# Optimization experiments

Hardware: AMD Instinct MI355X
Metric: run time of the kernel (lower is better)

Reference implementation:

```python
import jax, jax.numpy as jnp
import numpy as np
from jax import lax

B, L, D = 4, 4096, 1024
EXP = 2
DI = D * EXP
K_PERC = 7
KS_DIFF = 3
DILATIONS = (1, 4, 16)


def _dwconv(h, w, dil):
    # h: [B, C, L] channels-first, w: [C, 1, k] depthwise kernel (groups=C)
    k = w.shape[-1]
    pad = dil * (k // 2)
    return lax.conv_general_dilated(
        h, w, window_strides=(1,), padding=[(pad, pad)],
        rhs_dilation=(dil,), dimension_numbers=("NCH", "OIH", "NCH"),
        feature_group_count=w.shape[0])


def _layernorm(x, g, b, eps=1e-5):
    m = jnp.mean(x, axis=-1, keepdims=True)
    v = jnp.mean(jnp.square(x - m), axis=-1, keepdims=True)
    return (x - m) * lax.rsqrt(v + eps) * g + b


def setup_inputs() -> dict:
    key = jax.random.key(0)
    ks = jax.random.split(key, 16)
    n = lambda k, shape, scale: (jax.random.normal(k, shape, dtype=jnp.float32) * scale)
    inp = {
        "x": n(ks[0], (B, L, D), 1.0),
        # PerceptionFilter: 3 depthwise convs k=7, pointwise 3D->D, LayerNorm
        "pf_w0": n(ks[1], (D, 1, K_PERC), 0.3),
        "pf_w1": n(ks[2], (D, 1, K_PERC), 0.3),
        "pf_w2": n(ks[3], (D, 1, K_PERC), 0.3),
        "pf_pw": n(ks[4], (D, 3 * D), 1.0 / np.sqrt(3 * D)),
        "ln_g": jnp.ones((D,), jnp.float32),
        "ln_b": jnp.zeros((D,), jnp.float32),
        # ReactionGate: wu/wg: 2D->DI, wd: DI->D, alpha
        "rg_wu": n(ks[5], (DI, 2 * D), 1.0 / np.sqrt(2 * D)),
        "rg_wg": n(ks[6], (DI, 2 * D), 1.0 / np.sqrt(2 * D)),
        "rg_wd": n(ks[7], (D, DI), 1.0 / np.sqrt(DI)),
        "rg_alpha": jnp.full((D,), 0.1, jnp.float32),
        # MultiRateDiffusion: 3 depthwise dilated convs k=3, selector D->3, strength
        "md_w0": n(ks[8], (D, 1, KS_DIFF), 0.3),
        "md_w1": n(ks[9], (D, 1, KS_DIFF), 0.3),
        "md_w2": n(ks[10], (D, 1, KS_DIFF), 0.3),
        "md_sel": n(ks[11], (len(DILATIONS), D), 1.0 / np.sqrt(D)),
        "md_strength": jnp.asarray(0.1, jnp.float32),
    }
    return inp


def reference(x, pf_w0, pf_w1, pf_w2, pf_pw, ln_g, ln_b,
              rg_wu, rg_wg, rg_wd, rg_alpha,
              md_w0, md_w1, md_w2, md_sel, md_strength):
    # --- PerceptionFilter ---
    h = jnp.swapaxes(x, 1, 2)  # [B, D, L]
    pcat = jnp.concatenate([_dwconv(h, w, 1) for w in (pf_w0, pf_w1, pf_w2)], axis=1)  # [B, 3D, L]
    p = jnp.einsum("bcl,dc->bld", pcat, pf_pw)  # pointwise 1x1 conv -> [B, L, D]
    p = _layernorm(p, ln_g, ln_b)
    # --- ReactionGate ---
    cat = jnp.concatenate([x, p], axis=-1)  # [B, L, 2D]
    u = cat @ rg_wu.T
    g = jax.nn.sigmoid(cat @ rg_wg.T)
    x2 = x + rg_alpha * ((g * jax.nn.silu(u)) @ rg_wd.T)
    # --- MultiRateDiffusion ---
    h2 = jnp.swapaxes(x2, 1, 2)  # [B, D, L]
    diffs = jnp.stack([_dwconv(h2, w, dil) for w, dil in
                       zip((md_w0, md_w1, md_w2), DILATIONS)], axis=-1)  # [B, D, L, R]
    wsel = jax.nn.softmax(x2 @ md_sel.T, axis=-1)[:, None]  # [B, 1, L, R]
    combined = jnp.swapaxes(jnp.sum(diffs * wsel, axis=-1), 1, 2)  # [B, L, D]
    return x2 + md_strength * (combined - x2)
```

## Files before the change

### kernel.cpp

```cpp
#include <hip/hip_runtime.h>

#define LL 4096
#define BL 16384

typedef __attribute__((ext_vector_type(4))) float f32x4;
typedef __attribute__((ext_vector_type(4))) int i32x4;
typedef __attribute__((ext_vector_type(4))) unsigned short u16x4;
typedef __attribute__((ext_vector_type(2))) int i32x2;
typedef unsigned short ushort_t;
typedef unsigned int u32;

static __device__ __forceinline__ unsigned short f2bf(float f) {
    union { float f; unsigned int i; } v; v.f = f;
    unsigned int r = v.i + 0x7fffu + ((v.i >> 16) & 1u);
    return (unsigned short)(r >> 16);
}
static __device__ __forceinline__ float bf2f(unsigned short u) {
    union { unsigned int i; float f; } v; v.i = ((unsigned int)u) << 16; return v.f;
}
static __device__ __forceinline__ int qclamp(float x, float s) {
    return (int)rintf(fminf(fmaxf(x * s, -127.f), 127.f));
}
static __device__ __forceinline__ int q4(float a, float b, float c, float d, float s) {
    return (qclamp(a,s) & 255) | ((qclamp(b,s) & 255) << 8) |
           ((qclamp(c,s) & 255) << 16) | ((qclamp(d,s) & 255) << 24);
}

static __device__ __forceinline__ i32x4 mfma_i8(i32x4 a, i32x4 b, i32x4 c) {
    asm("v_mfma_i32_16x16x64_i8 %0, %1, %2, %0" : "+v"(c) : "v"(a), "v"(b));
    return c;
}

static __device__ __forceinline__ void gload16(const char* g, char* l) {
    __builtin_amdgcn_global_load_lds(
        (const __attribute__((address_space(1))) u32*)g,
        (__attribute__((address_space(3))) u32*)l, 16, 0, 0);
}

#define BAR()   asm volatile("s_barrier" ::: "memory")
#define VMW0()  asm volatile("s_waitcnt vmcnt(0)" ::: "memory")

__global__ void cvt_w8(const float* __restrict__ in, char* __restrict__ out,
                       int n4, float s) {
    int i = blockIdx.x * blockDim.x + threadIdx.x;
    int stride = gridDim.x * blockDim.x;
    for (; i < n4; i += stride) {
        f32x4 v = ((const f32x4*)in)[i];
        ((int*)out)[i] = q4(v[0], v[1], v[2], v[3], s);
    }
}

__global__ __launch_bounds__(256) void cvt_wug8(
    const float* __restrict__ wu, const float* __restrict__ wg,
    char* __restrict__ wug, float s)
{
    int r = blockIdx.x;
    int type = (r >> 4) & 1;
    int src = ((r >> 5) << 4) | (r & 15);
    const float* sp = (type ? wg : wu) + (size_t)src * 2048;
    char* d = wug + (size_t)r * 2048;
    int i = threadIdx.x;
    f32x4 v0 = ((const f32x4*)sp)[2 * i];
    f32x4 v1 = ((const f32x4*)sp)[2 * i + 1];
    i32x2 o = { q4(v0[0], v0[1], v0[2], v0[3], s),
                q4(v1[0], v1[1], v1[2], v1[3], s) };
    ((i32x2*)d)[i] = o;
}

__global__ __launch_bounds__(256) void pf_conv(
    const float* __restrict__ x,
    const float* __restrict__ w0, const float* __restrict__ w1, const float* __restrict__ w2,
    char* __restrict__ pcat, char* __restrict__ cat, float sP, float sX)
{
    int bl = blockIdx.x;
    int b = bl >> 12;
    int l = bl & 4095;
    int c0 = threadIdx.x << 2;

    f32x4 v[7];
#pragma unroll
    for (int t = 0; t < 7; ++t) {
        int ls = l + t - 3;
        if (ls >= 0 && ls < LL)
            v[t] = *(const f32x4*)(x + (((size_t)b * LL + ls) << 10) + c0);
        else {
            f32x4 z = {0.f, 0.f, 0.f, 0.f};
            v[t] = z;
        }
    }
    *(int*)(cat + (((size_t)bl) << 11) + c0) = q4(v[3][0], v[3][1], v[3][2], v[3][3], sX);
    const float* ww[3] = { w0, w1, w2 };
#pragma unroll
    for (int j = 0; j < 3; ++j) {
        const float* w = ww[j];
        float a[4];
#pragma unroll
        for (int e = 0; e < 4; ++e) {
            int c = c0 + e;
            float s = 0.f;
#pragma unroll
            for (int t = 0; t < 7; ++t) s += v[t][e] * w[c * 7 + t];
            a[e] = s;
        }
        *(int*)(pcat + (size_t)bl * 3072 + j * 1024 + c0) = q4(a[0], a[1], a[2], a[3], sP);
    }
}

__global__ __launch_bounds__(256) void ln_kernel(
    const ushort_t* __restrict__ p, const float* __restrict__ g,
    const float* __restrict__ bta, char* __restrict__ cat, float sX)
{
    int bl = blockIdx.x;
    int tid = threadIdx.x;
    int c0 = tid << 2;
    u16x4 pv = *(const u16x4*)(p + (((size_t)bl) << 10) + c0);
    float v0 = bf2f(pv[0]), v1 = bf2f(pv[1]), v2 = bf2f(pv[2]), v3 = bf2f(pv[3]);
    float s  = v0 + v1 + v2 + v3;
    float sq = v0*v0 + v1*v1 + v2*v2 + v3*v3;
#pragma unroll
    for (int off = 32; off > 0; off >>= 1) {
        s  += __shfl_down(s, off);
        sq += __shfl_down(sq, off);
    }
    __shared__ float rs[4], rq[4];
    int w = tid >> 6;
    if ((tid & 63) == 0) { rs[w] = s; rq[w] = sq; }
    __syncthreads();
    float S = rs[0] + rs[1] + rs[2] + rs[3];
    float Q = rq[0] + rq[1] + rq[2] + rq[3];
    float m   = S * (1.f / 1024.f);
    float var = Q * (1.f / 1024.f) - m * m;
    float inv = rsqrtf(var + 1e-5f);
    f32x4 gv = *(const f32x4*)(g + c0);
    f32x4 bv = *(const f32x4*)(bta + c0);
    *(int*)(cat + (((size_t)bl) << 11) + 1024 + c0) =
        q4((v0-m)*inv*gv[0]+bv[0], (v1-m)*inv*gv[1]+bv[1],
           (v2-m)*inv*gv[2]+bv[2], (v3-m)*inv*gv[3]+bv[3], sX);
}

template<int MODE>
__global__ __launch_bounds__(256, 3) void gemm8i(
    const char* __restrict__ A, const char* __restrict__ Bm,
    ushort_t* __restrict__ C16, char* __restrict__ C8,
    float* __restrict__ Cf, const float* __restrict__ X,
    const float* __restrict__ alpha,
    int N, int K, int lgny, float invS, float sOut)
{
    __shared__ char smem[32768];
    const int tid = threadIdx.x;
    const int wid = tid >> 6, lane = tid & 63;
    const int fr = lane & 15, fq = lane >> 4;
    const int wm = (wid >> 1) * 64;
    const int wn = (wid & 1) * 64;

    const int nwg = gridDim.x * gridDim.y;
    const int orig = blockIdx.y * gridDim.x + blockIdx.x;
    const int q = nwg >> 3;
    const int tile = (orig & 7) * q + (orig >> 3);
    const int m0 = (tile >> lgny) * 128;
    const int n0 = (tile & ((1 << lgny) - 1)) * 128;

    const int sp_ = tid >> 3;
    const int ss_ = tid & 7;
    const char* gp[4];
    int lpo[4];
#pragma unroll
    for (int op = 0; op < 2; ++op)
#pragma unroll
        for (int j = 0; j < 2; ++j) {
            int idx = op * 2 + j;
            const char* gs = op ? Bm : A;
            int rb = op ? n0 : m0;
            int p = j * 32 + sp_;
            int sh = ss_ ^ (p & 7);
            int r = 2 * p + (sh >> 2);
            int cch = sh & 3;
            gp[idx] = gs + (size_t)(rb + r) * K + cch * 16;
            lpo[idx] = op * 8192 + p * 128 + ss_ * 16;
        }

    const int lo = (fr >> 1) * 128 + (((((fr & 1) << 2) | fq)) ^ (fr >> 1)) * 16;
    const int arow = wm * 64 + lo;
    const int brow = 8192 + wn * 64 + lo;

    i32x4 acc[4][4] = {};
    const int NT = K >> 6;

#define STAGE(kt, s_) do {                                                  \
    _Pragma("unroll") for (int i_ = 0; i_ < 4; ++i_)                        \
        gload16(gp[i_] + (size_t)(kt) * 64, smem + (s_) * 16384 + lpo[i_]); \
    } while (0)

    STAGE(0, 0);
    VMW0();
    BAR();

    for (int t = 0; t < NT; ++t) {
        const int s = t & 1;
        const char* base = smem + s * 16384;
        const bool st = (t + 1 < NT);

        if (st) STAGE(t + 1, s ^ 1);

        i32x4 b[4], a[4];
#pragma unroll
        for (int n_ = 0; n_ < 4; ++n_) b[n_] = *(const i32x4*)(base + brow + n_ * 1024);
#pragma unroll
        for (int i_ = 0; i_ < 4; ++i_) a[i_] = *(const i32x4*)(base + arow + i_ * 1024);
        __builtin_amdgcn_s_setprio(1);
#pragma unroll
        for (int i_ = 0; i_ < 4; ++i_)
#pragma unroll
            for (int n_ = 0; n_ < 4; ++n_)
                acc[i_][n_] = mfma_i8(a[i_], b[n_], acc[i_][n_]);
        __builtin_amdgcn_s_setprio(0);

        if (st) VMW0();
        BAR();
    }
#undef STAGE

    const int mbase = m0 + wm + fq * 4;
#pragma unroll
    for (int mi = 0; mi < 4; ++mi) {
        if (MODE == 1) {
#pragma unroll
            for (int pi = 0; pi < 2; ++pi)
#pragma unroll
                for (int r = 0; r < 4; ++r) {
                    float u = (float)acc[mi][2 * pi][r] * invS;
                    float g = (float)acc[mi][2 * pi + 1][r] * invS;
                    float sg = 1.f / (1.f + __expf(-g));
                    float sl = u / (1.f + __expf(-u));
                    int col = ((n0 + wn) >> 1) + pi * 16 + fr;
                    C8[(size_t)(mbase + mi * 16 + r) * (N >> 1) + col] =
                        (char)qclamp(sg * sl, sOut);
                }
        } else {
#pragma unroll
            for (int ni = 0; ni < 4; ++ni)
#pragma unroll
                for (int r = 0; r < 4; ++r) {
                    int row = mbase + mi * 16 + r;
                    int col = n0 + wn + ni * 16 + fr;
                    size_t idx = (size_t)row * N + col;
                    float vv = (float)acc[mi][ni][r] * invS;
                    if (MODE == 0) C16[idx] = f2bf(vv);
                    else           Cf[idx] = X[idx] + alpha[col] * vv;
                }
        }
    }
}

__global__ __launch_bounds__(256) void diffusion(
    const float* __restrict__ x2,
    const float* __restrict__ w0, const float* __restrict__ w1, const float* __restrict__ w2,
    const float* __restrict__ sel, const float* __restrict__ strength_p,
    float* __restrict__ out)
{
    int bl = blockIdx.x;
    int b = bl >> 12;
    int l = bl & 4095;
    int tid = threadIdx.x;
    int c0 = tid << 2;
    const float* base = x2 + (((size_t)b * LL) << 10);

    f32x4 xc = *(const f32x4*)(x2 + (((size_t)bl) << 10) + c0);
    f32x4 s0 = *(const f32x4*)(sel + c0);
    f32x4 s1 = *(const f32x4*)(sel + 1024 + c0);
    f32x4 s2 = *(const f32x4*)(sel + 2048 + c0);
    float t0 = xc[0]*s0[0] + xc[1]*s0[1] + xc[2]*s0[2] + xc[3]*s0[3];
    float t1 = xc[0]*s1[0] + xc[1]*s1[1] + xc[2]*s1[2] + xc[3]*s1[3];
    float t2 = xc[0]*s2[0] + xc[1]*s2[1] + xc[2]*s2[2] + xc[3]*s2[3];
#pragma unroll
    for (int off = 32; off > 0; off >>= 1) {
        t0 += __shfl_down(t0, off);
        t1 += __shfl_down(t1, off);
        t2 += __shfl_down(t2, off);
    }
    __shared__ float r0[4], r1[4], r2[4];
    int w = tid >> 6;
    if ((tid & 63) == 0) { r0[w] = t0; r1[w] = t1; r2[w] = t2; }
    __syncthreads();
    float L0 = r0[0] + r0[1] + r0[2] + r0[3];
    float L1 = r1[0] + r1[1] + r1[2] + r1[3];
    float L2 = r2[0] + r2[1] + r2[2] + r2[3];
    float mx = fmaxf(L0, fmaxf(L1, L2));
    float e0 = __expf(L0 - mx), e1 = __expf(L1 - mx), e2 = __expf(L2 - mx);
    float inv = 1.f / (e0 + e1 + e2);
    float ws0 = e0 * inv, ws1 = e1 * inv, ws2 = e2 * inv;
    float stg = *strength_p;

    f32x4 comb = {0.f, 0.f, 0.f, 0.f};
    const float* wset[3] = { w0, w1, w2 };
    const int dils[3] = { 1, 4, 16 };
    const float wsel[3] = { ws0, ws1, ws2 };
#pragma unroll
    for (int r = 0; r < 3; ++r) {
        const float* wp = wset[r] + (size_t)c0 * 3;
        float wf[12];
        *(f32x4*)&wf[0] = *(const f32x4*)(wp + 0);
        *(f32x4*)&wf[4] = *(const f32x4*)(wp + 4);
        *(f32x4*)&wf[8] = *(const f32x4*)(wp + 8);
        int dil = dils[r];
        f32x4 d = {0.f, 0.f, 0.f, 0.f};
#pragma unroll
        for (int t = 0; t < 3; ++t) {
            int ls = l + (t - 1) * dil;
            f32x4 xv;
            if (ls >= 0 && ls < LL)
                xv = *(const f32x4*)(base + (((size_t)ls) << 10) + c0);
            else {
                f32x4 z = {0.f, 0.f, 0.f, 0.f};
                xv = z;
            }
#pragma unroll
            for (int e = 0; e < 4; ++e) d[e] += xv[e] * wf[e * 3 + t];
        }
#pragma unroll
        for (int e = 0; e < 4; ++e) comb[e] += wsel[r] * d[e];
    }
    f32x4 o;
#pragma unroll
    for (int e = 0; e < 4; ++e) o[e] = xc[e] + stg * (comb[e] - xc[e]);
    *(f32x4*)(out + (((size_t)bl) << 10) + c0) = o;
}

extern "C" void kernel_launch(void* const* d_in, const int* in_sizes, int n_in,
                              void* d_out, int out_size, void* d_ws, size_t ws_size,
                              hipStream_t stream)
{
    const float* x      = (const float*)d_in[0];
    const float* pf_w0  = (const float*)d_in[1];
    const float* pf_w1  = (const float*)d_in[2];
    const float* pf_w2  = (const float*)d_in[3];
    const float* pf_pw  = (const float*)d_in[4];
    const float* ln_g   = (const float*)d_in[5];
    const float* ln_b   = (const float*)d_in[6];
    const float* rg_wu  = (const float*)d_in[7];
    const float* rg_wg  = (const float*)d_in[8];
    const float* rg_wd  = (const float*)d_in[9];
    const float* rg_al  = (const float*)d_in[10];
    const float* md_w0  = (const float*)d_in[11];
    const float* md_w1  = (const float*)d_in[12];
    const float* md_w2  = (const float*)d_in[13];
    const float* md_sel = (const float*)d_in[14];
    const float* md_str = (const float*)d_in[15];
    float* outp = (float*)d_out;

    const float sP  = 127.f / 5.f;
    const float sX  = 127.f / 6.f;
    const float sW1 = 127.f / 0.11f;
    const float sW  = 127.f / 0.14f;
    const float invS1 = 1.f / (sP * sW1);
    const float invS2 = 1.f / (sX * sW);

    char* ws = (char*)d_ws;
    size_t off = 0;
    char*     pcat8 = (char*)   (ws + off); off += (size_t)BL * 3072;
    char*     cat8  = (char*)   (ws + off); off += (size_t)BL * 2048;
    ushort_t* ppre  = (ushort_t*)(ws + off); off += (size_t)BL * 1024 * 2;
    float*    x2    = (float*)  (ws + off); off += (size_t)BL * 1024 * 4;
    char*     wpw8  = (char*)   (ws + off); off += (size_t)1024 * 3072;
    char*     wug8  = (char*)   (ws + off); off += (size_t)4096 * 2048;
    char*     wd8   = (char*)   (ws + off); off += (size_t)1024 * 2048;
    char*     act8  = pcat8;

    cvt_w8<<<256, 256, 0, stream>>>(pf_pw, wpw8, 1024 * 3072 / 4, sW1);
    cvt_w8<<<256, 256, 0, stream>>>(rg_wd, wd8, 1024 * 2048 / 4, sW);
    cvt_wug8<<<4096, 256, 0, stream>>>(rg_wu, rg_wg, wug8, sW);

    pf_conv<<<BL, 256, 0, stream>>>(x, pf_w0, pf_w1, pf_w2, pcat8, cat8, sP, sX);

    gemm8i<0><<<dim3(128, 8), 256, 0, stream>>>(
        pcat8, wpw8, ppre, nullptr, nullptr, nullptr, nullptr, 1024, 3072, 3, invS1, 0.f);

    ln_kernel<<<BL, 256, 0, stream>>>(ppre, ln_g, ln_b, cat8, sX);

    gemm8i<1><<<dim3(128, 32), 256, 0, stream>>>(
        cat8, wug8, nullptr, act8, nullptr, nullptr, nullptr, 4096, 2048, 5, invS2, sX);

    gemm8i<2><<<dim3(128, 8), 256, 0, stream>>>(
        act8, wd8, nullptr, nullptr, x2, x, rg_al, 1024, 2048, 3, invS2, 0.f);

    diffusion<<<BL, 256, 0, stream>>>(x2, md_w0, md_w1, md_w2, md_sel, md_str, outp);
}
```

Before: 529.0 us.

## Double the int8 GEMM K-tile to 128 with a new swizzled LDS layout

The int8 MFMA GEMM now stages 128-wide K slices instead of 64, using 64KB of double-buffered LDS and a simpler XOR row swizzle. Each iteration runs two rounds of MFMA and halves the number of barriers and loop iterations. The cost is lower occupancy: launch bounds drop from 3 to 2 blocks per CU, and more LDS is used per block.

```diff
diff --git a/kernel.cpp b/kernel.cpp
--- a/kernel.cpp
+++ b/kernel.cpp
@@ -139,14 +139,14 @@
 }
 
 template<int MODE>
-__global__ __launch_bounds__(256, 3) void gemm8i(
+__global__ __launch_bounds__(256, 2) void gemm8i(
     const char* __restrict__ A, const char* __restrict__ Bm,
     ushort_t* __restrict__ C16, char* __restrict__ C8,
     float* __restrict__ Cf, const float* __restrict__ X,
     const float* __restrict__ alpha,
     int N, int K, int lgny, float invS, float sOut)
 {
-    __shared__ char smem[32768];
+    __shared__ char smem[65536];
     const int tid = threadIdx.x;
     const int wid = tid >> 6, lane = tid & 63;
     const int fr = lane & 15, fq = lane >> 4;
@@ -160,35 +160,32 @@
     const int m0 = (tile >> lgny) * 128;
     const int n0 = (tile & ((1 << lgny) - 1)) * 128;
 
-    const int sp_ = tid >> 3;
-    const int ss_ = tid & 7;
-    const char* gp[4];
-    int lpo[4];
+    const int srow = tid >> 3;
+    const int gch = ((tid & 7) ^ (srow & 7)) * 16;
+    const char* gp[8];
+    int lpo[8];
 #pragma unroll
     for (int op = 0; op < 2; ++op)
 #pragma unroll
-        for (int j = 0; j < 2; ++j) {
-            int idx = op * 2 + j;
+        for (int j = 0; j < 4; ++j) {
+            int idx = op * 4 + j;
             const char* gs = op ? Bm : A;
             int rb = op ? n0 : m0;
-            int p = j * 32 + sp_;
-            int sh = ss_ ^ (p & 7);
-            int r = 2 * p + (sh >> 2);
-            int cch = sh & 3;
-            gp[idx] = gs + (size_t)(rb + r) * K + cch * 16;
-            lpo[idx] = op * 8192 + p * 128 + ss_ * 16;
-        }
-
-    const int lo = (fr >> 1) * 128 + (((((fr & 1) << 2) | fq)) ^ (fr >> 1)) * 16;
-    const int arow = wm * 64 + lo;
-    const int brow = 8192 + wn * 64 + lo;
+            gp[idx] = gs + (size_t)(rb + j * 32 + srow) * K + gch;
+            lpo[idx] = op * 16384 + (j * 32 + srow) * 128 + (tid & 7) * 16;
+        }
+
+    const int ach0 = (fq ^ (fr & 7)) * 16;
+    const int ach1 = ((4 + fq) ^ (fr & 7)) * 16;
+    const int arow = (wm + fr) * 128;
+    const int brow = 16384 + (wn + fr) * 128;
 
     i32x4 acc[4][4] = {};
-    const int NT = K >> 6;
+    const int NT = K >> 7;
 
 #define STAGE(kt, s_) do {                                                  \
-    _Pragma("unroll") for (int i_ = 0; i_ < 4; ++i_)                        \
-        gload16(gp[i_] + (size_t)(kt) * 64, smem + (s_) * 16384 + lpo[i_]); \
+    _Pragma("unroll") for (int i_ = 0; i_ < 8; ++i_)                        \
+        gload16(gp[i_] + (size_t)(kt) * 128, smem + (s_) * 32768 + lpo[i_]);\
     } while (0)
 
     STAGE(0, 0);
@@ -197,16 +194,27 @@
 
     for (int t = 0; t < NT; ++t) {
         const int s = t & 1;
-        const char* base = smem + s * 16384;
+        const char* base = smem + s * 32768;
         const bool st = (t + 1 < NT);
 
         if (st) STAGE(t + 1, s ^ 1);
 
         i32x4 b[4], a[4];
 #pragma unroll
-        for (int n_ = 0; n_ < 4; ++n_) b[n_] = *(const i32x4*)(base + brow + n_ * 1024);
-#pragma unroll
-        for (int i_ = 0; i_ < 4; ++i_) a[i_] = *(const i32x4*)(base + arow + i_ * 1024);
+        for (int n_ = 0; n_ < 4; ++n_) b[n_] = *(const i32x4*)(base + brow + n_ * 2048 + ach0);
+#pragma unroll
+        for (int i_ = 0; i_ < 4; ++i_) a[i_] = *(const i32x4*)(base + arow + i_ * 2048 + ach0);
+        __builtin_amdgcn_s_setprio(1);
+#pragma unroll
+        for (int i_ = 0; i_ < 4; ++i_)
+#pragma unroll
+            for (int n_ = 0; n_ < 4; ++n_)
+                acc[i_][n_] = mfma_i8(a[i_], b[n_], acc[i_][n_]);
+        __builtin_amdgcn_s_setprio(0);
+#pragma unroll
+        for (int n_ = 0; n_ < 4; ++n_) b[n_] = *(const i32x4*)(base + brow + n_ * 2048 + ach1);
+#pragma unroll
+        for (int i_ = 0; i_ < 4; ++i_) a[i_] = *(const i32x4*)(base + arow + i_ * 2048 + ach1);
         __builtin_amdgcn_s_setprio(1);
 #pragma unroll
         for (int i_ = 0; i_ < 4; ++i_)
```

Result: faster. 495.0 us (-6.4%).
